# Kernel optimization log

Hardware: AMD Instinct MI355X
Metric: run time of the kernel (lower is better)

## Reference

```python
import jax, jax.numpy as jnp
import numpy as np

N, E, G = 50000, 1600000, 512
IN, H = 16, 128


def setup_inputs() -> dict:
    key = jax.random.key(0)
    ks = jax.random.split(key, 10)
    x = jax.random.normal(ks[0], (N, IN), dtype=jnp.float32)
    edge_index = jax.random.randint(ks[1], (2, E), 0, N, dtype=jnp.int64)
    batch = jnp.sort(jax.random.randint(ks[2], (N,), 0, G, dtype=jnp.int64))
    s = lambda k, sh, fan: jax.random.normal(k, sh, dtype=jnp.float32) / np.sqrt(fan)
    return {
        "x": x, "edge_index": edge_index, "batch": batch,
        "W1": s(ks[3], (IN, H), IN), "b1": jnp.zeros((H,), jnp.float32),
        "W2": s(ks[4], (H, H), H), "b2": jnp.zeros((H,), jnp.float32),
        "Wlab": s(ks[5], (H, 1), H), "blab": jnp.zeros((1,), jnp.float32),
        "Wd1": s(ks[6], (H, 64), H), "bd1": jnp.zeros((64,), jnp.float32),
        "Wd2": s(ks[7], (64, 2), 64), "bd2": jnp.zeros((2,), jnp.float32),
    }


def _gcn_conv(x, src, dst, norm, W, b, num_nodes):
    # x' = sum_{(s,d) in E+selfloops} norm_e * (x W)[s] scattered to d, + b
    h = x @ W                                  # [N, H]
    msgs = h[src] * norm[:, None]              # [E+N, H]
    out = jax.ops.segment_sum(msgs, dst, num_segments=num_nodes)
    return out + b


def _forward(x, edge_index, batch, W1, b1, W2, b2, Wlab, blab, Wd1, bd1, Wd2, bd2):
    num_nodes = x.shape[0]
    loop = jnp.arange(num_nodes, dtype=edge_index.dtype)
    src = jnp.concatenate([edge_index[0], loop])
    dst = jnp.concatenate([edge_index[1], loop])
    # symmetric GCN normalization: deg computed at dst after self-loops
    deg = jax.ops.segment_sum(jnp.ones_like(dst, dtype=x.dtype), dst,
                              num_segments=num_nodes)
    dinv = jnp.where(deg > 0, jax.lax.rsqrt(deg), 0.0)
    norm = dinv[src] * dinv[dst]               # [E+N]

    h = jax.nn.relu(_gcn_conv(x, src, dst, norm, W1, b1, num_nodes))
    h = jax.nn.relu(_gcn_conv(h, src, dst, norm, W2, b2, num_nodes))

    # global mean pool over graphs
    sums = jax.ops.segment_sum(h, batch, num_segments=G)        # [G, H]
    cnts = jax.ops.segment_sum(jnp.ones((num_nodes,), h.dtype), batch,
                               num_segments=G)
    pooled = sums / jnp.maximum(cnts, 1.0)[:, None]

    label_out = jax.nn.sigmoid(pooled @ Wlab + blab)            # [G, 1]
    # grad_reverse is identity in the forward pass
    dom_out = jax.nn.relu(pooled @ Wd1 + bd1) @ Wd2 + bd2       # [G, 2]
    return label_out, dom_out


def reference(x, edge_index, batch, W1, b1, W2, b2, Wlab, blab, Wd1, bd1, Wd2, bd2):
    return _forward(x, edge_index, batch, W1, b1, W2, b2, Wlab, blab,
                    Wd1, bd1, Wd2, bd2)
```

## Files before the change

kernel.cpp:

```cpp
#include <hip/hip_runtime.h>
#include <math.h>


#define BCAP 12288

typedef __attribute__((ext_vector_type(8))) short short8;
typedef __attribute__((ext_vector_type(4))) float f32x4;

__device__ __forceinline__ void bf4acc(uint2 u, float* a) {
    a[0] += __uint_as_float(u.x << 16);
    a[1] += __uint_as_float(u.x & 0xffff0000u);
    a[2] += __uint_as_float(u.y << 16);
    a[3] += __uint_as_float(u.y & 0xffff0000u);
}

__device__ __forceinline__ unsigned short bf1(float a) {
    unsigned ua = __float_as_uint(a);
    return (unsigned short)((ua + 0x7fffu + ((ua >> 16) & 1u)) >> 16);
}

__global__ __launch_bounds__(256) void k_bfill(
        const int* __restrict__ ei, int* __restrict__ bcnt,
        unsigned* __restrict__ col1,
        const int* __restrict__ batch, int* __restrict__ gptr,
        float* __restrict__ gsum, const float* __restrict__ W2,
        unsigned short* __restrict__ W2bf,
        int E, int chunk, int NB, int N, int G) {
    __shared__ int bins[256];
    __shared__ int base[256];
    for (int t = threadIdx.x; t < NB; t += 256) bins[t] = 0;
    __syncthreads();
    const int e0 = blockIdx.x * chunk;
    int e1 = e0 + chunk; if (e1 > E) e1 = E;
    for (int j = e0 + (int)threadIdx.x; j < e1; j += 256)
        atomicAdd(&bins[ei[E + j] >> 8], 1);
    __syncthreads();
    for (int t = threadIdx.x; t < NB; t += 256) {
        base[t] = bins[t] ? atomicAdd(&bcnt[t], bins[t]) : 0;
        bins[t] = 0;
    }
    __syncthreads();
    for (int j = e0 + (int)threadIdx.x; j < e1; j += 256) {
        int d = ei[E + j];
        int s = ei[j];
        int b = d >> 8;
        int pos = base[b] + atomicAdd(&bins[b], 1);
        if (pos < BCAP)
            col1[(size_t)b * BCAP + pos] = ((unsigned)(d & 255) << 16) | (unsigned)s;
    }

    const int gid = blockIdx.x * 256 + threadIdx.x;
    const int gsz = gridDim.x * 256;
    for (int i = gid; i < G * 32; i += gsz)
        ((float4*)gsum)[i] = make_float4(0.f, 0.f, 0.f, 0.f);
    for (int i = gid; i < 16384; i += gsz) {
        const int f2 = i >> 7, f1 = i & 127;
        W2bf[i] = bf1(W2[f1 * 128 + f2]);
    }
    for (int g = gid; g <= G; g += gsz) {
        int lo = 0, hi = N;
        while (lo < hi) {
            int mid = (lo + hi) >> 1;
            if (batch[mid] < g) lo = mid + 1; else hi = mid;
        }
        gptr[g] = lo;
    }
}

__global__ __launch_bounds__(256) void k_bsort(const unsigned* __restrict__ col1,
                                               const int* __restrict__ bcnt,
                                               int* __restrict__ col,
                                               int* __restrict__ rowptr,
                                               float* __restrict__ dinv,
                                               const float* __restrict__ x,
                                               unsigned short* __restrict__ xsb,
                                               int N, int E, int NB) {
    __shared__ unsigned ec[BCAP];
    __shared__ int bins[256], sc[256];
    __shared__ float dvb[256];
    const int b = blockIdx.x, t = threadIdx.x;

    {
        int v = (t < NB) ? bcnt[t] : 0;
        bins[t] = v;
        __syncthreads();
        for (int off = 1; off < 256; off <<= 1) {
            int add = (t >= off) ? bins[t - off] : 0;
            __syncthreads();
            bins[t] += add;
            __syncthreads();
        }
    }
    const int s0 = (b == 0) ? 0 : bins[b - 1];
    int cnt = bcnt[b];
    if (cnt > BCAP) cnt = BCAP;
    __syncthreads();

    for (int i = t; i < cnt; i += 256) ec[i] = col1[(size_t)b * BCAP + i];
    bins[t] = 0;
    __syncthreads();
    for (int i = t; i < cnt; i += 256) atomicAdd(&bins[ec[i] >> 16], 1);
    __syncthreads();
    const int v = bins[t];
    sc[t] = v;
    __syncthreads();
    for (int off = 1; off < 256; off <<= 1) {
        int add = (t >= off) ? sc[t - off] : 0;
        __syncthreads();
        sc[t] += add;
        __syncthreads();
    }
    const int ex = sc[t] - v;
    __syncthreads();
    sc[t] = ex;
    bins[t] = 0;
    const float dv = rsqrtf((float)(v + 1));
    dvb[t] = dv;
    const int n0 = b * 256;
    if (n0 + t < N) {
        rowptr[n0 + t] = s0 + ex;
        dinv[n0 + t] = dv;
    }
    if (b == 0 && t == 0) rowptr[N] = E;
    __syncthreads();
    for (int i = t; i < cnt; i += 256) {
        unsigned e = ec[i];
        int dl = e >> 16;
        int p = sc[dl] + atomicAdd(&bins[dl], 1);
        col[s0 + p] = (int)(e & 0xffffu);
    }
    int nn = N - n0; if (nn > 256) nn = 256;
    const int lim = nn * 16;
    for (int i = t; i < lim; i += 256) {
        float vx = x[(size_t)n0 * 16 + i] * dvb[i >> 4];
        xsb[(size_t)n0 * 16 + i] = bf1(vx);
    }
}

__global__ __launch_bounds__(512, 4) void k_l12g(
        const int* __restrict__ rowptr, const int* __restrict__ col,
        const unsigned short* __restrict__ xsb,
        const float* __restrict__ dinv,
        const float* __restrict__ W1, const float* __restrict__ b1,
        const unsigned short* __restrict__ W2bf,
        unsigned short* __restrict__ ht1b, int N) {
    __shared__ __align__(16) unsigned short W2s[128 * 136];
    __shared__ __align__(16) unsigned short h1b[64 * 136];
    __shared__ __align__(16) float arow[64 * 16];
    __shared__ float dv[64];
    const int tid = threadIdx.x;
    const int n0 = blockIdx.x * 64;
    const int w = tid >> 6, lane = tid & 63;

    for (int i = tid; i < 2048; i += 512) {
        const int f2 = i >> 4, seg = i & 15;
        *(uint4*)&W2s[f2 * 136 + seg * 8] = ((const uint4*)W2bf)[i];
    }
    if (tid < 64) dv[tid] = (n0 + tid < N) ? dinv[n0 + tid] : 0.f;

    {
        const int nd = lane >> 3, sub = lane & 7;
        const int slot = sub >> 2, qq = sub & 3;
        const int j = w * 8 + nd;
        const int n = n0 + j;
        float a[4] = {0.f, 0.f, 0.f, 0.f};
        if (n < N) {
            const int r1 = rowptr[n + 1];
            for (int e = rowptr[n] + slot; e < r1; e += 2)
                bf4acc(*(const uint2*)(xsb + (size_t)col[e] * 16 + qq * 4), a);
        }
#pragma unroll
        for (int i = 0; i < 4; ++i) a[i] += __shfl_xor(a[i], 4);
        if (slot == 0) {
            if (n < N) {
                bf4acc(*(const uint2*)(xsb + (size_t)n * 16 + qq * 4), a);
                *(float4*)&arow[j * 16 + qq * 4] = make_float4(a[0], a[1], a[2], a[3]);
            } else {
                *(float4*)&arow[j * 16 + qq * 4] = make_float4(0.f, 0.f, 0.f, 0.f);
            }
        }
    }
    const int f = tid & 127, jg = tid >> 7;
    float w1r[16];
#pragma unroll
    for (int k = 0; k < 16; ++k) w1r[k] = W1[k * 128 + f];
    const float bias = b1[f];
    __syncthreads();

#pragma unroll 4
    for (int j = jg * 16; j < jg * 16 + 16; ++j) {
        float s = 0.f;
#pragma unroll
        for (int k = 0; k < 16; ++k) s += arow[j * 16 + k] * w1r[k];
        h1b[j * 136 + f] = bf1(fmaxf(dv[j] * s + bias, 0.f));
    }
    __syncthreads();

    const int mt = w & 3, nh = w >> 2;
    const int lm = lane & 15, quad = lane >> 4;
    f32x4 acc[4];
#pragma unroll
    for (int t = 0; t < 4; ++t) acc[t] = (f32x4){0.f, 0.f, 0.f, 0.f};
#pragma unroll
    for (int kb = 0; kb < 4; ++kb) {
        const short8 af = *(const short8*)&h1b[(mt * 16 + lm) * 136 + kb * 32 + quad * 8];
#pragma unroll
        for (int t = 0; t < 4; ++t) {
            const short8 bfv = *(const short8*)&W2s[(nh * 64 + t * 16 + lm) * 136 + kb * 32 + quad * 8];
            acc[t] = __builtin_amdgcn_mfma_f32_16x16x32_bf16(af, bfv, acc[t], 0, 0, 0);
        }
    }
#pragma unroll
    for (int t = 0; t < 4; ++t) {
        const int f2 = nh * 64 + t * 16 + lm;
#pragma unroll
        for (int r = 0; r < 4; ++r) {
            const int j = mt * 16 + quad * 4 + r;
            const int n = n0 + j;
            if (n < N)
                ht1b[(size_t)n * 128 + f2] = bf1(acc[t][r] * dv[j]);
        }
    }
}

__global__ __launch_bounds__(512) void k_gat128pool(
        const int* __restrict__ rowptr, const int* __restrict__ col,
        const unsigned short* __restrict__ ht1b,
        const float* __restrict__ dinv, const float* __restrict__ b2,
        const int* __restrict__ batch, float* __restrict__ gsum, int N) {
    __shared__ __align__(16) float h2s[8][128];
    __shared__ int bats[8];
    const int wave = threadIdx.x >> 6, lane = threadIdx.x & 63;
    const int half = lane >> 5, q = lane & 31;
    const int n = blockIdx.x * 8 + wave;
    float a[4] = {0.f, 0.f, 0.f, 0.f};
    if (n < N) {
        const int r0 = rowptr[n], r1 = rowptr[n + 1];
        int j = r0 + half;
        while (j + 6 < r1) {
            int s0 = col[j], s1 = col[j + 2], s2 = col[j + 4], s3 = col[j + 6];
            uint2 u0 = *(const uint2*)(ht1b + (size_t)s0 * 128 + q * 4);
            uint2 u1 = *(const uint2*)(ht1b + (size_t)s1 * 128 + q * 4);
            uint2 u2 = *(const uint2*)(ht1b + (size_t)s2 * 128 + q * 4);
            uint2 u3 = *(const uint2*)(ht1b + (size_t)s3 * 128 + q * 4);
            bf4acc(u0, a); bf4acc(u1, a); bf4acc(u2, a); bf4acc(u3, a);
            j += 8;
        }
        while (j < r1) {
            bf4acc(*(const uint2*)(ht1b + (size_t)col[j] * 128 + q * 4), a);
            j += 2;
        }
        if (half == 0)
            bf4acc(*(const uint2*)(ht1b + (size_t)n * 128 + q * 4), a);
    }
#pragma unroll
    for (int i = 0; i < 4; ++i) a[i] += __shfl_xor(a[i], 32);
    if (half == 0) {
        if (n < N) {
            const float d = dinv[n];
            const float4 bb = *(const float4*)(b2 + q * 4);
            h2s[wave][q * 4 + 0] = fmaxf(a[0] * d + bb.x, 0.f);
            h2s[wave][q * 4 + 1] = fmaxf(a[1] * d + bb.y, 0.f);
            h2s[wave][q * 4 + 2] = fmaxf(a[2] * d + bb.z, 0.f);
            h2s[wave][q * 4 + 3] = fmaxf(a[3] * d + bb.w, 0.f);
            if (q == 0) bats[wave] = batch[n];
        } else {
            h2s[wave][q * 4 + 0] = 0.f; h2s[wave][q * 4 + 1] = 0.f;
            h2s[wave][q * 4 + 2] = 0.f; h2s[wave][q * 4 + 3] = 0.f;
            if (q == 0) bats[wave] = -1;
        }
    }
    __syncthreads();
    if (threadIdx.x < 32) {
        const int qq = threadIdx.x;
        int bprev = bats[0];
        float4 acc4 = *(const float4*)&h2s[0][qq * 4];
#pragma unroll
        for (int wv = 1; wv < 8; ++wv) {
            const int bw = bats[wv];
            const float4 rv = *(const float4*)&h2s[wv][qq * 4];
            if (bw == bprev) {
                acc4.x += rv.x; acc4.y += rv.y; acc4.z += rv.z; acc4.w += rv.w;
            } else {
                if (bprev >= 0) {
                    float* gs = gsum + (size_t)bprev * 128 + qq * 4;
                    unsafeAtomicAdd(gs + 0, acc4.x); unsafeAtomicAdd(gs + 1, acc4.y);
                    unsafeAtomicAdd(gs + 2, acc4.z); unsafeAtomicAdd(gs + 3, acc4.w);
                }
                bprev = bw; acc4 = rv;
            }
        }
        if (bprev >= 0) {
            float* gs = gsum + (size_t)bprev * 128 + qq * 4;
            unsafeAtomicAdd(gs + 0, acc4.x); unsafeAtomicAdd(gs + 1, acc4.y);
            unsafeAtomicAdd(gs + 2, acc4.z); unsafeAtomicAdd(gs + 3, acc4.w);
        }
    }
}

__global__ __launch_bounds__(128) void k_head(
        const float* __restrict__ gsum, const int* __restrict__ gptr,
        const float* __restrict__ Wlab, const float* __restrict__ blab,
        const float* __restrict__ Wd1, const float* __restrict__ bd1,
        const float* __restrict__ Wd2, const float* __restrict__ bd2,
        float* __restrict__ out, int G) {
    __shared__ float sp[128];
    __shared__ float red[128];
    __shared__ float hd[64];
    const int g = blockIdx.x, t = threadIdx.x;
    const float cnt = (float)(gptr[g + 1] - gptr[g]);
    const float invc = 1.f / fmaxf(cnt, 1.f);
    const float pooled = gsum[g * 128 + t] * invc;
    sp[t] = pooled;
    red[t] = pooled * Wlab[t];
    __syncthreads();
    for (int off = 64; off > 0; off >>= 1) {
        if (t < off) red[t] += red[t + off];
        __syncthreads();
    }
    if (t == 0) {
        float z = red[0] + blab[0];
        out[g] = 1.f / (1.f + expf(-z));
    }
    if (t < 64) {
        float s = bd1[t];
        for (int f = 0; f < 128; ++f) s += sp[f] * Wd1[f * 64 + t];
        hd[t] = fmaxf(s, 0.f);
    }
    __syncthreads();
    if (t < 2) {
        float s = bd2[t];
        for (int j = 0; j < 64; ++j) s += hd[j] * Wd2[j * 2 + t];
        out[G + g * 2 + t] = s;
    }
}

extern "C" void kernel_launch(void* const* d_in, const int* in_sizes, int n_in,
                              void* d_out, int out_size, void* d_ws, size_t ws_size,
                              hipStream_t stream) {
    const float* x     = (const float*)d_in[0];
    const int*   ei    = (const int*)d_in[1];
    const int*   batch = (const int*)d_in[2];
    const float* W1    = (const float*)d_in[3];
    const float* b1    = (const float*)d_in[4];
    const float* W2    = (const float*)d_in[5];
    const float* b2    = (const float*)d_in[6];
    const float* Wlab  = (const float*)d_in[7];
    const float* blab  = (const float*)d_in[8];
    const float* Wd1   = (const float*)d_in[9];
    const float* bd1   = (const float*)d_in[10];
    const float* Wd2   = (const float*)d_in[11];
    const float* bd2   = (const float*)d_in[12];
    float* out = (float*)d_out;

    const int N = in_sizes[0] / 16;
    const int E = in_sizes[1] / 2;
    const int G = out_size / 3;
    const int NB = (N + 255) >> 8;

    char* p = (char*)d_ws;
    auto carve = [&](size_t bytes) {
        void* r = (void*)p;
        p += (bytes + 255) & ~(size_t)255;
        return r;
    };
    int*      bcnt   = (int*)     carve(256 * 4);
    unsigned* col1   = (unsigned*)carve((size_t)NB * BCAP * 4);
    int*      col    = (int*)     carve((size_t)E * 4);
    int*      rowptr = (int*)     carve((size_t)(N + 1) * 4);
    int*      gptr   = (int*)     carve((size_t)(G + 1) * 4);
    float*    dinv   = (float*)   carve((size_t)N * 4);
    unsigned short* xsb  = (unsigned short*)carve((size_t)N * 16 * 2);
    unsigned short* W2bf = (unsigned short*)carve(128 * 128 * 2);
    unsigned short* ht1b = (unsigned short*)carve((size_t)N * 128 * 2);
    float*    gsum   = (float*)   carve((size_t)G * 128 * 4);

    const int FB = 256;
    const int chunk = (E + FB - 1) / FB;

    hipMemsetAsync(bcnt, 0, 256 * 4, stream);
    k_bfill  <<<FB, 256, 0, stream>>>(ei, bcnt, col1, batch, gptr, gsum, W2,
                                      W2bf, E, chunk, NB, N, G);
    k_bsort  <<<NB, 256, 0, stream>>>(col1, bcnt, col, rowptr, dinv, x, xsb,
                                      N, E, NB);
    k_l12g   <<<(N + 63) / 64, 512, 0, stream>>>(rowptr, col, xsb, dinv,
                                                 W1, b1, W2bf, ht1b, N);
    k_gat128pool<<<(N + 7) / 8, 512, 0, stream>>>(rowptr, col, ht1b, dinv, b2,
                                                  batch, gsum, N);
    k_head   <<<G, 128, 0, stream>>>(gsum, gptr, Wlab, blab, Wd1, bd1, Wd2,
                                     bd2, out, G);
}
```

Baseline: 229.8 us.

## Split per-bucket CSR sort across four blocks per bucket quarter

The bucket sort kernel now launches four blocks per 256-node bucket, each handling a 64-node quarter. Each block re-reads the whole bucket from global memory, counts edges below its quarter to find its base offset, and scatters only its own edges, dropping the large shared-memory staging buffer. This raises block count and occupancy for the CSR build at the cost of reading each bucket four times and doing extra reductions.

```diff
diff --git a/kernel.cpp b/kernel.cpp
--- a/kernel.cpp
+++ b/kernel.cpp
@@ -67,7 +67,7 @@
     }
 }
 
-__global__ __launch_bounds__(256) void k_bsort(const unsigned* __restrict__ col1,
+__global__ __launch_bounds__(256) void k_qsort(const unsigned* __restrict__ col1,
                                                const int* __restrict__ bcnt,
                                                int* __restrict__ col,
                                                int* __restrict__ rowptr,
@@ -75,65 +75,83 @@
                                                const float* __restrict__ x,
                                                unsigned short* __restrict__ xsb,
                                                int N, int E, int NB) {
-    __shared__ unsigned ec[BCAP];
-    __shared__ int bins[256], sc[256];
-    __shared__ float dvb[256];
+    __shared__ int bins[64], sc[64];
+    __shared__ int red[256];
+    __shared__ float dvb[64];
     const int b = blockIdx.x, t = threadIdx.x;
-
-    {
-        int v = (t < NB) ? bcnt[t] : 0;
-        bins[t] = v;
+    const int parent = b >> 2, qlo = (b & 3) << 6;
+
+    int part = 0;
+    for (int i = t; i < parent; i += 256) part += bcnt[i];
+    red[t] = part;
+    __syncthreads();
+    for (int off = 128; off > 0; off >>= 1) {
+        if (t < off) red[t] += red[t + off];
         __syncthreads();
-        for (int off = 1; off < 256; off <<= 1) {
-            int add = (t >= off) ? bins[t - off] : 0;
-            __syncthreads();
-            bins[t] += add;
-            __syncthreads();
-        }
-    }
-    const int s0 = (b == 0) ? 0 : bins[b - 1];
-    int cnt = bcnt[b];
-    if (cnt > BCAP) cnt = BCAP;
-    __syncthreads();
-
-    for (int i = t; i < cnt; i += 256) ec[i] = col1[(size_t)b * BCAP + i];
-    bins[t] = 0;
-    __syncthreads();
-    for (int i = t; i < cnt; i += 256) atomicAdd(&bins[ec[i] >> 16], 1);
-    __syncthreads();
-    const int v = bins[t];
-    sc[t] = v;
-    __syncthreads();
-    for (int off = 1; off < 256; off <<= 1) {
-        int add = (t >= off) ? sc[t - off] : 0;
+    }
+    const int s0p = red[0];
+    int pcnt = bcnt[parent];
+    if (pcnt > BCAP) pcnt = BCAP;
+    if (t < 64) bins[t] = 0;
+    __syncthreads();
+
+    const unsigned* srcp = col1 + (size_t)parent * BCAP;
+    int lc = 0;
+    for (int i = t; i < pcnt; i += 256) {
+        const int dl = (int)(srcp[i] >> 16);
+        const int r = dl - qlo;
+        if ((unsigned)r < 64u) atomicAdd(&bins[r], 1);
+        else if (dl < qlo) ++lc;
+    }
+    red[t] = lc;
+    __syncthreads();
+    for (int off = 128; off > 0; off >>= 1) {
+        if (t < off) red[t] += red[t + off];
         __syncthreads();
-        sc[t] += add;
+    }
+    const int lowcnt = red[0];
+
+    if (t < 64) sc[t] = bins[t];
+    __syncthreads();
+    for (int off = 1; off < 64; off <<= 1) {
+        int add = (t >= off && t < 64) ? sc[t - off] : 0;
         __syncthreads();
-    }
-    const int ex = sc[t] - v;
-    __syncthreads();
-    sc[t] = ex;
-    bins[t] = 0;
-    const float dv = rsqrtf((float)(v + 1));
-    dvb[t] = dv;
-    const int n0 = b * 256;
-    if (n0 + t < N) {
-        rowptr[n0 + t] = s0 + ex;
-        dinv[n0 + t] = dv;
+        if (t < 64) sc[t] += add;
+        __syncthreads();
+    }
+    const int base = s0p + lowcnt;
+    const int n0 = parent * 256 + qlo;
+    if (t < 64) {
+        const int v = bins[t];
+        const int ex = sc[t] - v;
+        sc[t] = ex;
+        bins[t] = 0;
+        const float dv = rsqrtf((float)(v + 1));
+        dvb[t] = dv;
+        if (n0 + t < N) {
+            rowptr[n0 + t] = base + ex;
+            dinv[n0 + t] = dv;
+        }
     }
     if (b == 0 && t == 0) rowptr[N] = E;
     __syncthreads();
-    for (int i = t; i < cnt; i += 256) {
-        unsigned e = ec[i];
-        int dl = e >> 16;
-        int p = sc[dl] + atomicAdd(&bins[dl], 1);
-        col[s0 + p] = (int)(e & 0xffffu);
-    }
-    int nn = N - n0; if (nn > 256) nn = 256;
-    const int lim = nn * 16;
-    for (int i = t; i < lim; i += 256) {
-        float vx = x[(size_t)n0 * 16 + i] * dvb[i >> 4];
-        xsb[(size_t)n0 * 16 + i] = bf1(vx);
+
+    for (int i = t; i < pcnt; i += 256) {
+        const unsigned e = srcp[i];
+        const int r = (int)(e >> 16) - qlo;
+        if ((unsigned)r < 64u) {
+            const int p = sc[r] + atomicAdd(&bins[r], 1);
+            col[base + p] = (int)(e & 0xffffu);
+        }
+    }
+    int nn = N - n0;
+    if (nn > 64) nn = 64;
+    if (nn > 0) {
+        const int lim = nn * 16;
+        for (int i = t; i < lim; i += 256) {
+            float vx = x[(size_t)n0 * 16 + i] * dvb[i >> 4];
+            xsb[(size_t)n0 * 16 + i] = bf1(vx);
+        }
     }
 }
 
@@ -381,8 +399,8 @@
     hipMemsetAsync(bcnt, 0, 256 * 4, stream);
     k_bfill  <<<FB, 256, 0, stream>>>(ei, bcnt, col1, batch, gptr, gsum, W2,
                                       W2bf, E, chunk, NB, N, G);
-    k_bsort  <<<NB, 256, 0, stream>>>(col1, bcnt, col, rowptr, dinv, x, xsb,
-                                      N, E, NB);
+    k_qsort  <<<NB * 4, 256, 0, stream>>>(col1, bcnt, col, rowptr, dinv, x,
+                                          xsb, N, E, NB);
     k_l12g   <<<(N + 63) / 64, 512, 0, stream>>>(rowptr, col, xsb, dinv,
                                                  W1, b1, W2bf, ht1b, N);
     k_gat128pool<<<(N + 7) / 8, 512, 0, stream>>>(rowptr, col, ht1b, dinv, b2,
```

After: 245.4 us. 1.07x slower.
